# Kernel optimization log

Measured on AMD Instinct MI355X. Metric: run time of the kernel, lower is better.

Reference implementation:

```python
import jax, jax.numpy as jnp
import numpy as np

N = 10000          # num nodes == num_api
C = 128            # api_embed_channels
E = 320000         # num edges


def _mlp(x, w1, b1, w2, b2):
    # MLP.forward: elu(fc1) -> dropout(eval: identity) -> elu(fc2). BN method is never called.
    return jax.nn.elu(jax.nn.elu(x @ w1 + b1) @ w2 + b2)


def setup_inputs() -> dict:
    key = jax.random.key(0)
    ks = jax.random.split(key, 24)
    r = lambda i, shape, s: (jax.random.normal(ks[i], shape, jnp.float32) * s)
    d = {}
    d['api_embeds'] = r(0, (N, C), 1.0)
    d['adjacency_matrix'] = jax.random.uniform(ks[1], (N, N), jnp.float32)
    d['edge_index'] = jax.random.randint(ks[2], (2, E), 0, N, jnp.int64)
    # reduce_mlp (dead code in original forward, kept for signature parity)
    d['w_red1'] = r(3, (N, 3 * C), 0.01);  d['b_red1'] = jnp.full((3 * C,), 0.1, jnp.float32)
    d['w_red2'] = r(4, (3 * C, C), 0.05);  d['b_red2'] = jnp.full((C,), 0.1, jnp.float32)
    # Node2Node.mlp1: MLP(4C, 2C, 2C)
    d['w_m1a'] = r(5, (4 * C, 2 * C), 0.05); d['b_m1a'] = jnp.full((2 * C,), 0.1, jnp.float32)
    d['w_m1b'] = r(6, (2 * C, 2 * C), 0.05); d['b_m1b'] = jnp.full((2 * C,), 0.1, jnp.float32)
    # Node2Node.mlp2: MLP(2C, 2C, 2C)
    d['w_m2a'] = r(7, (2 * C, 2 * C), 0.05); d['b_m2a'] = jnp.full((2 * C,), 0.1, jnp.float32)
    d['w_m2b'] = r(8, (2 * C, 2 * C), 0.05); d['b_m2b'] = jnp.full((2 * C,), 0.1, jnp.float32)
    # AdaptiveNRI.mlp: MLP(2C, 2C, 2C)
    d['w_ma'] = r(9, (2 * C, 2 * C), 0.05);  d['b_ma'] = jnp.full((2 * C,), 0.1, jnp.float32)
    d['w_mb'] = r(10, (2 * C, 2 * C), 0.05); d['b_mb'] = jnp.full((2 * C,), 0.1, jnp.float32)
    # increase_mlp: Linear(C, 3C) -> ReLU -> Linear(3C, N) -> Sigmoid
    d['w_inc1'] = r(11, (C, 3 * C), 0.05);   d['b_inc1'] = jnp.full((3 * C,), 0.1, jnp.float32)
    d['w_inc2'] = r(12, (3 * C, N), 0.05);   d['b_inc2'] = jnp.full((N,), 0.1, jnp.float32)
    return d


def reference(api_embeds, adjacency_matrix, edge_index,
              w_red1, b_red1, w_red2, b_red2,
              w_m1a, b_m1a, w_m1b, b_m1b,
              w_m2a, b_m2a, w_m2b, b_m2b,
              w_ma, b_ma, w_mb, b_mb,
              w_inc1, b_inc1, w_inc2, b_inc2):
    # NOTE: in the original torch code, reduce_mlp(adjacency_matrix) is computed and
    # immediately overwritten (dead code) -> adjacency does not affect the output.
    x = jnp.concatenate([api_embeds, api_embeds], axis=1)          # [N, 2C]
    src = edge_index[0]   # x_j (source)
    dst = edge_index[1]   # x_i (target, aggregation index)
    # message: MLP1(cat[x_i, x_j]) per edge -> [E, 2C]
    msg = _mlp(jnp.concatenate([x[dst], x[src]], axis=-1), w_m1a, b_m1a, w_m1b, b_m1b)
    # aggregate: scatter-add at targets
    agg = jax.ops.segment_sum(msg, dst, num_segments=N)            # [N, 2C]
    # update: MLP2
    h = _mlp(agg, w_m2a, b_m2a, w_m2b, b_m2b)                      # [N, 2C]
    h = _mlp(h, w_ma, b_ma, w_mb, b_mb)                            # [N, 2C]
    h = h[:, -C:]                                                  # [N, C]
    out = jax.nn.sigmoid(jax.nn.relu(h @ w_inc1 + b_inc1) @ w_inc2 + b_inc2)  # [N, N]
    return out
```

## Files before the change

### kernel.cpp

```cpp
#include <hip/hip_runtime.h>

#define DEVI __device__ __forceinline__

typedef __attribute__((ext_vector_type(8))) short short8;
typedef __attribute__((ext_vector_type(4))) short short4v;
typedef __attribute__((ext_vector_type(4))) float f32x4;
typedef unsigned short u16;
typedef unsigned int u32;

DEVI float b2f(u16 u) { u32 x = ((u32)u) << 16; return __builtin_bit_cast(float, x); }
DEVI u16 f2b(float f) {
    u32 u = __builtin_bit_cast(u32, f);
    u32 r = u + 0x7FFFu + ((u >> 16) & 1u);
    return (u16)(r >> 16);
}
DEVI float eluf(float v) { return v > 0.f ? v : __expf(v) - 1.f; }

DEVI void gl16(const void* g, void* l) {
    __builtin_amdgcn_global_load_lds(
        (const __attribute__((address_space(1))) u32*)g,
        (__attribute__((address_space(3))) u32*)l, 16, 0, 0);
}

__global__ void k_prep(const float* __restrict__ api, u16* __restrict__ e16,
                       const float* __restrict__ w_m1a, u16* __restrict__ wct,
                       const float* __restrict__ w1b, const float* __restrict__ w2a,
                       const float* __restrict__ w2b, const float* __restrict__ wa,
                       const float* __restrict__ wb,
                       u16* __restrict__ t1b, u16* __restrict__ t2a, u16* __restrict__ t2b,
                       u16* __restrict__ ta, u16* __restrict__ tb,
                       const float* __restrict__ w_inc1, u16* __restrict__ i1T,
                       const float* __restrict__ w_inc2, u16* __restrict__ i2T,
                       const int* __restrict__ ei, int* __restrict__ hist) {
    __shared__ float tile[32][33];
    const int b = blockIdx.x, tid = threadIdx.x;
    const int E = 320000;

    if (b < 625) {
        int base = (b * 256 + tid) * 8;
        float4 a = *(const float4*)(api + base);
        float4 c = *(const float4*)(api + base + 4);
        short8 o;
        o[0] = (short)f2b(a.x); o[1] = (short)f2b(a.y);
        o[2] = (short)f2b(a.z); o[3] = (short)f2b(a.w);
        o[4] = (short)f2b(c.x); o[5] = (short)f2b(c.y);
        o[6] = (short)f2b(c.z); o[7] = (short)f2b(c.w);
        *(short8*)(e16 + base) = o;
    } else if (b < 881) {
        int t = (b - 625) * 256 + tid;
        int k = t & 127, j = t >> 7;
        float v;
        if (j < 256) v = w_m1a[k * 256 + j] + w_m1a[(k + 128) * 256 + j];
        else { int jj = j - 256; v = w_m1a[(k + 256) * 256 + jj] + w_m1a[(k + 384) * 256 + jj]; }
        wct[j * 128 + k] = f2b(v);
    } else if (b < 5089) {
        const float* w; u16* wt; int K, Nn, Nalloc, bx, by;
        if (b < 1201) {
            int idx = b - 881, wi = idx >> 6, blk = idx & 63;
            switch (wi) {
                case 0: w = w1b; wt = t1b; break;
                case 1: w = w2a; wt = t2a; break;
                case 2: w = w2b; wt = t2b; break;
                case 3: w = wa;  wt = ta;  break;
                default: w = wb; wt = tb;  break;
            }
            K = 256; Nn = 256; Nalloc = 256; bx = blk & 7; by = blk >> 3;
        } else if (b < 1249) {
            int idx = b - 1201;
            w = w_inc1; wt = i1T; K = 128; Nn = 384; Nalloc = 384;
            bx = idx % 12; by = idx / 12;
        } else {
            int idx = b - 1249;
            w = w_inc2; wt = i2T; K = 384; Nn = 10000; Nalloc = 10240;
            bx = idx % 320; by = idx / 320;
        }
        int tx = tid & 31, ty = tid >> 5;
        int k0 = by * 32, n0 = bx * 32;
#pragma unroll
        for (int yy = 0; yy < 4; ++yy) {
            int k = k0 + ty + yy * 8, n = n0 + tx;
            tile[ty + yy * 8][tx] = (k < K && n < Nn) ? w[(size_t)k * Nn + n] : 0.f;
        }
        __syncthreads();
#pragma unroll
        for (int yy = 0; yy < 4; ++yy) {
            int n = n0 + ty + yy * 8, k = k0 + tx;
            if (n < Nalloc && k < K) wt[(size_t)n * K + k] = f2b(tile[tx][ty + yy * 8]);
        }
    } else {
        int i = (b - 5089) * 256 + tid;
        if (i < E) atomicAdd(&hist[ei[E + i]], 1);
    }
}

__global__ void k_scan(const int* __restrict__ hist, int* __restrict__ cursor, int NB) {
    __shared__ int part[256];
    int t = threadIdx.x;
    int base = t * 40;
    int s = 0;
    for (int i = 0; i < 40; ++i) { int idx = base + i; if (idx < NB) s += hist[idx]; }
    part[t] = s;
    __syncthreads();
    if (t == 0) { int run = 0; for (int i = 0; i < 256; ++i) { int x = part[i]; part[i] = run; run += x; } }
    __syncthreads();
    int run = part[t];
    for (int i = 0; i < 40; ++i) {
        int idx = base + i;
        if (idx < NB) { int h = hist[idx]; cursor[idx] = run; run += h; }
    }
}

__global__ void k_scatter(const int* __restrict__ ei, int* __restrict__ cursor,
                          int* __restrict__ sdst, int* __restrict__ ssrc, int E) {
    int i = blockIdx.x * 256 + threadIdx.x;
    if (i >= E) return;
    int d = ei[E + i], s = ei[i];
    int pos = atomicAdd(&cursor[d], 1);
    sdst[pos] = d;
    ssrc[pos] = s;
}

__global__ __launch_bounds__(256, 2)
void k_gemm(const u16* __restrict__ A, const u16* __restrict__ BT,
            void* __restrict__ Cv, int M, int N, int K, int lda, int ldbt, int ldc) {
    __shared__ short lsA[128 * 64];
    __shared__ short lsB[128 * 64];
    const int tid = threadIdx.x, wave = tid >> 6, lane = tid & 63;
    const int m0 = blockIdx.y * 128, n0 = blockIdx.x * 128;
    const int wm = wave >> 1, wn = wave & 1;
    const int rowA = lane >> 3, colA = (lane & 7) * 8;

    f32x4 acc[4][4] = {};

    const int kch = K >> 6;
    for (int kc = 0; kc < kch; ++kc) {
#pragma unroll
        for (int i = 0; i < 4; ++i) {
            int slot = wave * 4 + i;
            const u16* ga = A + (size_t)(m0 + slot * 8 + rowA) * lda + kc * 64 + colA;
            gl16(ga, &lsA[slot * 512]);
            const u16* gb = BT + (size_t)(n0 + slot * 8 + rowA) * ldbt + kc * 64 + colA;
            gl16(gb, &lsB[slot * 512]);
        }
        __syncthreads();
#pragma unroll
        for (int ks = 0; ks < 2; ++ks) {
            short8 a[4], b[4];
#pragma unroll
            for (int m = 0; m < 4; ++m)
                a[m] = *(const short8*)&lsA[(wm * 64 + m * 16 + (lane & 15)) * 64 + ks * 32 + (lane >> 4) * 8];
#pragma unroll
            for (int n = 0; n < 4; ++n)
                b[n] = *(const short8*)&lsB[(wn * 64 + n * 16 + (lane & 15)) * 64 + ks * 32 + (lane >> 4) * 8];
#pragma unroll
            for (int m = 0; m < 4; ++m)
#pragma unroll
                for (int n = 0; n < 4; ++n)
                    acc[m][n] = __builtin_amdgcn_mfma_f32_16x16x32_bf16(a[m], b[n], acc[m][n], 0, 0, 0);
        }
        __syncthreads();
    }

#pragma unroll
    for (int m = 0; m < 4; ++m) {
#pragma unroll
        for (int n = 0; n < 4; ++n) {
            int colg = n0 + wn * 64 + n * 16 + (lane & 15);
#pragma unroll
            for (int j = 0; j < 4; ++j) {
                int rowg = m0 + wm * 64 + m * 16 + (lane >> 4) * 4 + j;
                if (rowg < M && colg < N)
                    ((u16*)Cv)[(size_t)rowg * ldc + colg] = f2b(acc[m][n][j]);
            }
        }
    }
}

__global__ __launch_bounds__(512, 4)
void k_gemm2(const u16* __restrict__ A, const u16* __restrict__ BT,
             const float* __restrict__ bias, float* __restrict__ C,
             int M, int N, int K, int lda, int ldbt, int ldc) {
    __shared__ short lsA[256 * 64];
    __shared__ short lsB[128 * 64];
    const int tid = threadIdx.x, wave = tid >> 6, lane = tid & 63;
    const int g = lane >> 4, l15 = lane & 15;
    const int orig = blockIdx.x;
    const int wg = (orig & 7) * 395 + (orig >> 3);
    const int x = wg / 395;
    const int l = wg - x * 395;
    int bxl, byl;
    if (l < 360) { int sc = l / 40, r = l - sc * 40; int q = r / 5; bxl = sc * 8 + q; byl = r - q * 5; }
    else         { int r = l - 360;                   int q = r / 5; bxl = 72 + q;     byl = r - q * 5; }
    const int bx = bxl, by = x * 5 + byl;
    const int m0 = by * 256, n0 = bx * 128;
    const int wm = wave >> 1, wn = wave & 1;
    const int sr = lane >> 3, sc2 = lane & 7;

    f32x4 acc[4][4] = {};
    const int kch = K >> 6;
    for (int kc = 0; kc < kch; ++kc) {
#pragma unroll
        for (int i = 0; i < 4; ++i) {
            int s = wave * 4 + i;
            int br = s * 8 + sr;
            const u16* ga = A + (size_t)(m0 + br) * lda + kc * 64 + ((sc2 ^ (br & 7)) * 8);
            gl16(ga, &lsA[s * 512]);
        }
#pragma unroll
        for (int i = 0; i < 2; ++i) {
            int s = wave * 2 + i;
            int br = s * 8 + sr;
            const u16* gb = BT + (size_t)(n0 + br) * ldbt + kc * 64 + ((sc2 ^ (br & 7)) * 8);
            gl16(gb, &lsB[s * 512]);
        }
        __syncthreads();
#pragma unroll
        for (int ks = 0; ks < 2; ++ks) {
            short8 a[4], b[4];
#pragma unroll
            for (int m = 0; m < 4; ++m) {
                int ar = wm * 64 + m * 16 + l15;
                a[m] = *(const short8*)&lsA[(ar * 8 + ((ks * 4 + g) ^ (ar & 7))) * 8];
            }
#pragma unroll
            for (int n = 0; n < 4; ++n) {
                int br = wn * 64 + n * 16 + l15;
                b[n] = *(const short8*)&lsB[(br * 8 + ((ks * 4 + g) ^ (br & 7))) * 8];
            }
#pragma unroll
            for (int m = 0; m < 4; ++m)
#pragma unroll
                for (int n = 0; n < 4; ++n)
                    acc[m][n] = __builtin_amdgcn_mfma_f32_16x16x32_bf16(b[n], a[m], acc[m][n], 0, 0, 0);
        }
        __syncthreads();
    }

#pragma unroll
    for (int m = 0; m < 4; ++m) {
        int row = m0 + wm * 64 + m * 16 + l15;
        if (row < M) {
#pragma unroll
            for (int n = 0; n < 4; ++n) {
                int col0 = n0 + wn * 64 + n * 16 + g * 4;
                if (col0 < N) {
                    float4 bv = *(const float4*)(bias + col0);
                    f32x4 o;
                    o[0] = 1.f / (1.f + __expf(-(acc[m][n][0] + bv.x)));
                    o[1] = 1.f / (1.f + __expf(-(acc[m][n][1] + bv.y)));
                    o[2] = 1.f / (1.f + __expf(-(acc[m][n][2] + bv.z)));
                    o[3] = 1.f / (1.f + __expf(-(acc[m][n][3] + bv.w)));
                    __builtin_nontemporal_store(o, (f32x4*)(C + (size_t)row * ldc + col0));
                }
            }
        }
    }
}

__global__ __launch_bounds__(256, 2)
void k_chain(const float* __restrict__ agg,
             const u16* __restrict__ w2aT, const float* __restrict__ b_m2a,
             const u16* __restrict__ w2bT, const float* __restrict__ b_m2b,
             const u16* __restrict__ waT,  const float* __restrict__ b_ma,
             const u16* __restrict__ wbT,  const float* __restrict__ b_mb,
             const u16* __restrict__ i1T,  const float* __restrict__ b_inc1,
             u16* __restrict__ H1, int M) {
    __shared__ short lsX[32 * 256];
    __shared__ short lsW[384 * 64];
    const int tid = threadIdx.x, wave = tid >> 6, lane = tid & 63;
    const int g = lane >> 4, l15 = lane & 15;
    const int r0 = blockIdx.x * 32;

    for (int c = tid; c < 2048; c += 256) {
        int row = c >> 6, cg = c & 63;
        int grow = r0 + row;
        float4 v = (grow < M) ? *(const float4*)(agg + (size_t)grow * 256 + cg * 4)
                              : float4{0.f, 0.f, 0.f, 0.f};
        short4v o;
        o[0] = (short)f2b(v.x); o[1] = (short)f2b(v.y);
        o[2] = (short)f2b(v.z); o[3] = (short)f2b(v.w);
        *(short4v*)&lsX[row * 256 + (((cg >> 1) ^ (row & 7)) * 8 + (cg & 1) * 4)] = o;
    }

    auto do_layer = [&](const u16* WT, const float* bias) {
        f32x4 acc[2][4] = {};
        for (int kc = 0; kc < 4; ++kc) {
#pragma unroll
            for (int i = 0; i < 8; ++i) {
                int slot = wave * 8 + i;
                int br = slot * 8 + (lane >> 3);
                const u16* gw = WT + (size_t)br * 256 + kc * 64 + (((lane & 7) ^ (br & 7)) * 8);
                gl16(gw, &lsW[slot * 512]);
            }
            __syncthreads();
#pragma unroll
            for (int ks = 0; ks < 2; ++ks) {
                short8 a[2], b[4];
#pragma unroll
                for (int m = 0; m < 2; ++m) {
                    int ar = m * 16 + l15;
                    a[m] = *(const short8*)&lsX[ar * 256 + (kc * 8 + ((ks * 4 + g) ^ (ar & 7))) * 8];
                }
#pragma unroll
                for (int n = 0; n < 4; ++n) {
                    int br = wave * 64 + n * 16 + l15;
                    b[n] = *(const short8*)&lsW[(br * 8 + ((ks * 4 + g) ^ (br & 7))) * 8];
                }
#pragma unroll
                for (int m = 0; m < 2; ++m)
#pragma unroll
                    for (int n = 0; n < 4; ++n)
                        acc[m][n] = __builtin_amdgcn_mfma_f32_16x16x32_bf16(b[n], a[m], acc[m][n], 0, 0, 0);
            }
            __syncthreads();
        }
#pragma unroll
        for (int m = 0; m < 2; ++m) {
#pragma unroll
            for (int n = 0; n < 4; ++n) {
                int row = m * 16 + l15;
                int col0 = wave * 64 + n * 16 + g * 4;
                float4 bv = *(const float4*)(bias + col0);
                short4v o;
                o[0] = (short)f2b(eluf(acc[m][n][0] + bv.x));
                o[1] = (short)f2b(eluf(acc[m][n][1] + bv.y));
                o[2] = (short)f2b(eluf(acc[m][n][2] + bv.z));
                o[3] = (short)f2b(eluf(acc[m][n][3] + bv.w));
                int cg = col0 >> 2;
                *(short4v*)&lsX[row * 256 + (((cg >> 1) ^ (row & 7)) * 8 + (cg & 1) * 4)] = o;
            }
        }
        __syncthreads();
    };

    do_layer(w2aT, b_m2a);
    do_layer(w2bT, b_m2b);
    do_layer(waT,  b_ma);
    do_layer(wbT,  b_mb);

    f32x4 acc2[2][6] = {};
    for (int kc = 0; kc < 2; ++kc) {
#pragma unroll
        for (int i = 0; i < 12; ++i) {
            int slot = wave * 12 + i;
            int br = slot * 8 + (lane >> 3);
            const u16* gw = i1T + (size_t)br * 128 + kc * 64 + (((lane & 7) ^ (br & 7)) * 8);
            gl16(gw, &lsW[slot * 512]);
        }
        __syncthreads();
#pragma unroll
        for (int ks = 0; ks < 2; ++ks) {
            short8 a[2], b[6];
#pragma unroll
            for (int m = 0; m < 2; ++m) {
                int ar = m * 16 + l15;
                a[m] = *(const short8*)&lsX[ar * 256 + (16 + kc * 8 + ((ks * 4 + g) ^ (ar & 7))) * 8];
            }
#pragma unroll
            for (int n = 0; n < 6; ++n) {
                int br = wave * 96 + n * 16 + l15;
                b[n] = *(const short8*)&lsW[(br * 8 + ((ks * 4 + g) ^ (br & 7))) * 8];
            }
#pragma unroll
            for (int m = 0; m < 2; ++m)
#pragma unroll
                for (int n = 0; n < 6; ++n)
                    acc2[m][n] = __builtin_amdgcn_mfma_f32_16x16x32_bf16(b[n], a[m], acc2[m][n], 0, 0, 0);
        }
        __syncthreads();
    }
#pragma unroll
    for (int m = 0; m < 2; ++m) {
        int grow = r0 + m * 16 + l15;
        if (grow < M) {
#pragma unroll
            for (int n = 0; n < 6; ++n) {
                int col0 = wave * 96 + n * 16 + g * 4;
                float4 bv = *(const float4*)(b_inc1 + col0);
                float v0 = acc2[m][n][0] + bv.x, v1 = acc2[m][n][1] + bv.y;
                float v2 = acc2[m][n][2] + bv.z, v3 = acc2[m][n][3] + bv.w;
                short4v o;
                o[0] = (short)f2b(v0 > 0.f ? v0 : 0.f);
                o[1] = (short)f2b(v1 > 0.f ? v1 : 0.f);
                o[2] = (short)f2b(v2 > 0.f ? v2 : 0.f);
                o[3] = (short)f2b(v3 > 0.f ? v3 : 0.f);
                *(short4v*)&H1[(size_t)grow * 384 + col0] = o;
            }
        }
    }
}

__global__ __launch_bounds__(256, 2)
void k_edge(const u16* __restrict__ P, const int* __restrict__ sdst,
            const int* __restrict__ ssrc, const float* __restrict__ b1,
            const u16* __restrict__ W2T, const float* __restrict__ b2,
            float* __restrict__ agg) {
    __shared__ __align__(16) char smem[49152];
    __shared__ int dstl[128];
    __shared__ int srcl[128];
    short* lsA = (short*)smem;
    short* lsB = (short*)(smem + 16384);
    float* lsO = (float*)smem;
    const int tid = threadIdx.x, wave = tid >> 6, lane = tid & 63;
    const int eb = blockIdx.x * 128;
    const int g = lane >> 4, l15 = lane & 15;

    if (tid < 128) srcl[tid] = ssrc[eb + tid];
    else dstl[tid - 128] = sdst[eb + (tid - 128)];
    __syncthreads();

    short8 rpd[4], rps[4];
    auto loadA = [&](int kc) {
#pragma unroll
        for (int it = 0; it < 4; ++it) {
            int chunk = it * 256 + tid;
            int r = chunk >> 3, cc = chunk & 7;
            int col = kc * 64 + cc * 8;
            rpd[it] = *(const short8*)(P + (size_t)dstl[r] * 512 + col);
            rps[it] = *(const short8*)(P + (size_t)srcl[r] * 512 + 256 + col);
        }
    };

    loadA(0);
    f32x4 acc[4][2][4] = {};

    for (int kc = 0; kc < 4; ++kc) {
#pragma unroll
        for (int it = 0; it < 4; ++it) {
            int chunk = it * 256 + tid;
            int r = chunk >> 3, cc = chunk & 7;
            int col = kc * 64 + cc * 8;
            float bv[8];
            *(float4*)&bv[0] = *(const float4*)(b1 + col);
            *(float4*)&bv[4] = *(const float4*)(b1 + col + 4);
            short8 o;
#pragma unroll
            for (int jj = 0; jj < 8; ++jj) {
                float v = b2f((u16)rpd[it][jj]) + b2f((u16)rps[it][jj]) + bv[jj];
                o[jj] = (short)f2b(eluf(v));
            }
            int ccs = cc ^ (r & 7);
            *(short8*)&lsA[(r * 8 + ccs) * 8] = o;
        }
#pragma unroll
        for (int i = 0; i < 8; ++i) {
            int br = (wave * 8 + i) * 8 + (lane >> 3);
            const u16* gb = W2T + (size_t)br * 256 + kc * 64 + (((lane & 7) ^ (br & 7)) * 8);
            gl16(gb, lsB + (wave * 8 + i) * 512);
        }
        __syncthreads();
        if (kc < 3) loadA(kc + 1);
        short8 af[2][2];
#pragma unroll
        for (int ks = 0; ks < 2; ++ks)
#pragma unroll
            for (int m = 0; m < 2; ++m) {
                int ar = wave * 32 + m * 16 + l15;
                af[ks][m] = *(const short8*)&lsA[(ar * 8 + ((ks * 4 + g) ^ (ar & 7))) * 8];
            }
#pragma unroll
        for (int nq = 0; nq < 4; ++nq) {
#pragma unroll
            for (int ks = 0; ks < 2; ++ks) {
                short8 b[4];
#pragma unroll
                for (int n = 0; n < 4; ++n) {
                    int br = nq * 64 + n * 16 + l15;
                    b[n] = *(const short8*)&lsB[(br * 8 + ((ks * 4 + g) ^ (br & 7))) * 8];
                }
#pragma unroll
                for (int m = 0; m < 2; ++m)
#pragma unroll
                    for (int n = 0; n < 4; ++n)
                        acc[nq][m][n] = __builtin_amdgcn_mfma_f32_16x16x32_bf16(af[ks][m], b[n], acc[nq][m][n], 0, 0, 0);
            }
        }
        __syncthreads();
    }

    const int r0w = wave * 32;
    const int dls = dstl[r0w + (lane & 31)];

#pragma unroll
    for (int nq = 0; nq < 4; ++nq) {
        float b2v[4];
#pragma unroll
        for (int n = 0; n < 4; ++n) b2v[n] = b2[nq * 64 + n * 16 + l15];
#pragma unroll
        for (int m = 0; m < 2; ++m)
#pragma unroll
            for (int n = 0; n < 4; ++n)
#pragma unroll
                for (int j = 0; j < 4; ++j) {
                    int row = r0w + m * 16 + g * 4 + j;
                    lsO[row * 68 + n * 16 + l15] = eluf(acc[nq][m][n][j] + b2v[n]);
                }
        {
            int dprev = __builtin_amdgcn_readlane(dls, 0);
            float sum = 0.f;
#pragma unroll
            for (int i = 0; i < 32; ++i) {
                int d = __builtin_amdgcn_readlane(dls, i);
                float v = lsO[(r0w + i) * 68 + lane];
                if (d != dprev) {
                    atomicAdd(&agg[(size_t)dprev * 256 + nq * 64 + lane], sum);
                    sum = v; dprev = d;
                } else sum += v;
            }
            atomicAdd(&agg[(size_t)dprev * 256 + nq * 64 + lane], sum);
        }
    }
}

extern "C" void kernel_launch(void* const* d_in, const int* in_sizes, int n_in,
                              void* d_out, int out_size, void* d_ws, size_t ws_size,
                              hipStream_t stream) {
    const float* api    = (const float*)d_in[0];
    const int*   ei     = (const int*)d_in[2];
    const float* w_m1a  = (const float*)d_in[7];
    const float* b_m1a  = (const float*)d_in[8];
    const float* w_m1b  = (const float*)d_in[9];
    const float* b_m1b  = (const float*)d_in[10];
    const float* w_m2a  = (const float*)d_in[11];
    const float* b_m2a  = (const float*)d_in[12];
    const float* w_m2b  = (const float*)d_in[13];
    const float* b_m2b  = (const float*)d_in[14];
    const float* w_ma   = (const float*)d_in[15];
    const float* b_ma   = (const float*)d_in[16];
    const float* w_mb   = (const float*)d_in[17];
    const float* b_mb   = (const float*)d_in[18];
    const float* w_inc1 = (const float*)d_in[19];
    const float* b_inc1 = (const float*)d_in[20];
    const float* w_inc2 = (const float*)d_in[21];
    const float* b_inc2 = (const float*)d_in[22];

    const int N = 10000, C = 128, E = 320000, Mp = 10112;
    const int Mp2 = 10240;

    char* w = (char*)d_ws;
    size_t off = 0;
    auto alloc = [&](size_t bytes) { void* p = w + off; off += (bytes + 255) & ~(size_t)255; return p; };
    u16* e16   = (u16*)alloc((size_t)Mp * 128 * 2);
    u16* WcT   = (u16*)alloc(512 * 128 * 2);
    u16* P     = (u16*)alloc((size_t)Mp * 512 * 2);
    u16* w1bT  = (u16*)alloc(256 * 256 * 2);
    u16* w2aT  = (u16*)alloc(256 * 256 * 2);
    u16* w2bT  = (u16*)alloc(256 * 256 * 2);
    u16* waT   = (u16*)alloc(256 * 256 * 2);
    u16* wbT   = (u16*)alloc(256 * 256 * 2);
    u16* i1T   = (u16*)alloc(384 * 128 * 2);
    u16* i2T   = (u16*)alloc((size_t)Mp2 * 384 * 2);
    float* agg = (float*)alloc((size_t)N * 256 * 4);
    u16* H1    = (u16*)alloc((size_t)Mp2 * 384 * 2);
    int* hist  = (int*)alloc((size_t)N * 4);
    int* cursor= (int*)alloc((size_t)N * 4);
    int* sdst  = (int*)alloc((size_t)E * 4);
    int* ssrc  = (int*)alloc((size_t)E * 4);
    (void)ws_size; (void)in_sizes; (void)n_in; (void)out_size;

    hipMemsetAsync(hist, 0, (size_t)N * 4, stream);
    hipMemsetAsync(agg, 0, (size_t)N * 256 * 4, stream);

    k_prep<<<6339, 256, 0, stream>>>(api, e16, w_m1a, WcT,
                                     w_m1b, w_m2a, w_m2b, w_ma, w_mb,
                                     w1bT, w2aT, w2bT, waT, wbT,
                                     w_inc1, i1T, w_inc2, i2T, ei, hist);
    k_scan<<<1, 256, 0, stream>>>(hist, cursor, N);
    k_scatter<<<1250, 256, 0, stream>>>(ei, cursor, sdst, ssrc, E);

    k_gemm<<<dim3(4, 79), 256, 0, stream>>>(e16, WcT, P, N, 512, 128, 128, 128, 512);
    k_edge<<<2500, 256, 0, stream>>>(P, sdst, ssrc, b_m1a, w1bT, b_m1b, agg);
    k_chain<<<313, 256, 0, stream>>>(agg, w2aT, b_m2a, w2bT, b_m2b,
                                     waT, b_ma, wbT, b_mb, i1T, b_inc1, H1, N);
    k_gemm2<<<3160, 512, 0, stream>>>(H1, i2T, b_inc2, (float*)d_out,
                                      N, 10000, 384, 384, 384, 10000);
}
```

Measured before the change: 382.2 us.

## Double-buffer LDS in final sigmoid GEMM with 32-wide K chunks

The output GEMM kernel now splits LDS into two buffers of 32-wide K slices and prefetches the next slice with global_load_lds while MFMAs run on the current one. This removes the load-then-wait stall that came from a single buffer with two barriers per iteration. The K chunk is halved and the swizzle pattern changes to match the new row width, so there are more loop iterations and barriers per unit of work, while total LDS size stays the same.

```diff
diff --git a/kernel.cpp b/kernel.cpp
--- a/kernel.cpp
+++ b/kernel.cpp
@@ -180,8 +180,8 @@
 void k_gemm2(const u16* __restrict__ A, const u16* __restrict__ BT,
              const float* __restrict__ bias, float* __restrict__ C,
              int M, int N, int K, int lda, int ldbt, int ldc) {
-    __shared__ short lsA[256 * 64];
-    __shared__ short lsB[128 * 64];
+    __shared__ short lsA[2][256 * 32];
+    __shared__ short lsB[2][128 * 32];
     const int tid = threadIdx.x, wave = tid >> 6, lane = tid & 63;
     const int g = lane >> 4, l15 = lane & 15;
     const int orig = blockIdx.x;
@@ -194,46 +194,51 @@
     const int bx = bxl, by = x * 5 + byl;
     const int m0 = by * 256, n0 = bx * 128;
     const int wm = wave >> 1, wn = wave & 1;
-    const int sr = lane >> 3, sc2 = lane & 7;
-
-    f32x4 acc[4][4] = {};
-    const int kch = K >> 6;
-    for (int kc = 0; kc < kch; ++kc) {
-#pragma unroll
-        for (int i = 0; i < 4; ++i) {
-            int s = wave * 4 + i;
-            int br = s * 8 + sr;
-            const u16* ga = A + (size_t)(m0 + br) * lda + kc * 64 + ((sc2 ^ (br & 7)) * 8);
-            gl16(ga, &lsA[s * 512]);
-        }
+    const int srow = lane >> 2, schk = lane & 3;
+
+    auto stage = [&](int buf, int kc) {
 #pragma unroll
         for (int i = 0; i < 2; ++i) {
             int s = wave * 2 + i;
-            int br = s * 8 + sr;
-            const u16* gb = BT + (size_t)(n0 + br) * ldbt + kc * 64 + ((sc2 ^ (br & 7)) * 8);
-            gl16(gb, &lsB[s * 512]);
-        }
-        __syncthreads();
-#pragma unroll
-        for (int ks = 0; ks < 2; ++ks) {
-            short8 a[4], b[4];
-#pragma unroll
-            for (int m = 0; m < 4; ++m) {
-                int ar = wm * 64 + m * 16 + l15;
-                a[m] = *(const short8*)&lsA[(ar * 8 + ((ks * 4 + g) ^ (ar & 7))) * 8];
-            }
-#pragma unroll
-            for (int n = 0; n < 4; ++n) {
-                int br = wn * 64 + n * 16 + l15;
-                b[n] = *(const short8*)&lsB[(br * 8 + ((ks * 4 + g) ^ (br & 7))) * 8];
-            }
-#pragma unroll
-            for (int m = 0; m < 4; ++m)
-#pragma unroll
-                for (int n = 0; n < 4; ++n)
-                    acc[m][n] = __builtin_amdgcn_mfma_f32_16x16x32_bf16(b[n], a[m], acc[m][n], 0, 0, 0);
-        }
-        __syncthreads();
+            int row = s * 16 + srow;
+            const u16* ga = A + (size_t)(m0 + row) * lda + kc * 32
+                          + ((schk ^ ((row >> 1) & 3)) * 8);
+            gl16(ga, &lsA[buf][s * 512]);
+        }
+        {
+            int s = wave;
+            int row = s * 16 + srow;
+            const u16* gb = BT + (size_t)(n0 + row) * ldbt + kc * 32
+                          + ((schk ^ ((row >> 1) & 3)) * 8);
+            gl16(gb, &lsB[buf][s * 512]);
+        }
+    };
+
+    f32x4 acc[4][4] = {};
+    const int kch = K >> 5;
+    stage(0, 0);
+    __syncthreads();
+    int cur = 0;
+    for (int kc = 0; kc < kch; ++kc) {
+        if (kc + 1 < kch) stage(cur ^ 1, kc + 1);
+        short8 a[4], b[4];
+#pragma unroll
+        for (int m = 0; m < 4; ++m) {
+            int ar = wm * 64 + m * 16 + l15;
+            a[m] = *(const short8*)&lsA[cur][ar * 32 + ((g ^ ((ar >> 1) & 3)) * 8)];
+        }
+#pragma unroll
+        for (int n = 0; n < 4; ++n) {
+            int br = wn * 64 + n * 16 + l15;
+            b[n] = *(const short8*)&lsB[cur][br * 32 + ((g ^ ((br >> 1) & 3)) * 8)];
+        }
+#pragma unroll
+        for (int m = 0; m < 4; ++m)
+#pragma unroll
+            for (int n = 0; n < 4; ++n)
+                acc[m][n] = __builtin_amdgcn_mfma_f32_16x16x32_bf16(b[n], a[m], acc[m][n], 0, 0, 0);
+        __syncthreads();
+        cur ^= 1;
     }
 
 #pragma unroll
```

New measurement: 390.7 us. 1.02x slower.
